# Kernel optimization log

Measured on AMD Instinct MI355X. Metric: run time of the kernel, lower is better.

The kernel has to match this reference:

```python
import jax, jax.numpy as jnp
import numpy as np

V, D, NH, L, HID, E, K = 32000, 1024, 16, 2, 2048, 8, 2
B, S = 2, 1024
HD = D // NH
EPS = 1e-6
ROPE_BASE = 10000.0


def setup_inputs() -> dict:
    key = jax.random.key(0)
    ks = jax.random.split(key, 12)
    s = 0.02
    return {
        "tokens": jax.random.randint(ks[0], (B, S), 0, V),
        "embed": jax.random.normal(ks[1], (V, D), jnp.float32) * s,
        "attn_norm_w": jnp.ones((L, D), jnp.float32),
        "wq": jax.random.normal(ks[2], (L, D, D), jnp.float32) * s,
        "wk": jax.random.normal(ks[3], (L, D, D), jnp.float32) * s,
        "wv": jax.random.normal(ks[4], (L, D, D), jnp.float32) * s,
        "wo": jax.random.normal(ks[5], (L, D, D), jnp.float32) * s,
        "moe_norm_w": jnp.ones((L, D), jnp.float32),
        "router_w": jax.random.normal(ks[6], (L, E, D), jnp.float32) * s,
        "w1": jax.random.normal(ks[7], (L, E, D, HID), jnp.float32) * s,
        "w2": jax.random.normal(ks[8], (L, E, HID, D), jnp.float32) * s,
        "w3": jax.random.normal(ks[9], (L, E, D, HID), jnp.float32) * s,
        "final_norm_w": jnp.ones((D,), jnp.float32),
    }


def rmsnorm(x, w):
    var = jnp.mean(jnp.square(x), axis=-1, keepdims=True)
    return x * jax.lax.rsqrt(var + EPS) * w


def rope(x):  # x: [B, S, NH, HD], rotate-half convention
    half = HD // 2
    inv = ROPE_BASE ** (-jnp.arange(half, dtype=jnp.float32) / half)
    ang = jnp.arange(x.shape[1], dtype=jnp.float32)[:, None] * inv[None, :]  # [S, half]
    cos = jnp.cos(ang)[None, :, None, :]
    sin = jnp.sin(ang)[None, :, None, :]
    x1, x2 = x[..., :half], x[..., half:]
    return jnp.concatenate([x1 * cos - x2 * sin, x1 * sin + x2 * cos], axis=-1)


def attention(x, wq, wk, wv, wo):
    q = (x @ wq).reshape(B, S, NH, HD)
    k = (x @ wk).reshape(B, S, NH, HD)
    v = (x @ wv).reshape(B, S, NH, HD)
    q, k = rope(q), rope(k)
    scores = jnp.einsum("bqhd,bkhd->bhqk", q, k) / jnp.sqrt(jnp.float32(HD))
    mask = jnp.tril(jnp.ones((S, S), bool))
    scores = jnp.where(mask[None, None], scores, jnp.finfo(scores.dtype).min)
    attn = jax.nn.softmax(scores, axis=-1)
    ctx = jnp.einsum("bhqk,bkhd->bqhd", attn, v).reshape(B, S, D)
    return ctx @ wo


def moe(x, router_w, w1, w2, w3):
    flat = x.reshape(-1, D)                      # [T, D]
    T = flat.shape[0]
    logits = flat @ router_w.T                   # [T, E]
    topv, topi = jax.lax.top_k(logits, K)
    topw = jax.nn.softmax(topv, axis=-1)         # softmax over selected logits
    gates = jnp.zeros((T, E), flat.dtype).at[jnp.arange(T)[:, None], topi].set(topw)
    out = jnp.zeros_like(flat)
    for e in range(E):  # small fixed expert count; gates are exact-sparse so math == dispatch path
        y = (jax.nn.silu(flat @ w1[e]) * (flat @ w3[e])) @ w2[e]
        out = out + y * gates[:, e:e + 1]
    return out.reshape(x.shape)


def reference(tokens, embed, attn_norm_w, wq, wk, wv, wo, moe_norm_w,
              router_w, w1, w2, w3, final_norm_w):
    x = embed[tokens]  # [B, S, D]
    for l in range(L):
        x = x + attention(rmsnorm(x, attn_norm_w[l]), wq[l], wk[l], wv[l], wo[l])
        x = x + moe(rmsnorm(x, moe_norm_w[l]), router_w[l], w1[l], w2[l], w3[l])
    x = rmsnorm(x, final_norm_w)
    return x @ embed.T  # tied logits [B, S, V]
```

## Files before the change

kernel.cpp:

```cpp
#include <hip/hip_runtime.h>
#include <math.h>

typedef unsigned short u16;
typedef unsigned int u32;
typedef __attribute__((ext_vector_type(8))) short bf16x8;
typedef __attribute__((ext_vector_type(4))) float f32x4;

#define TOK 2048
#define SEQ 1024
#define DM 1024
#define NEXP 8
#define VOCAB 32000
#define NL 2
#define SLOTS 5120
#define APAD 40

__device__ __forceinline__ float bf2f(u16 v) {
  u32 u = ((u32)v) << 16; float f; __builtin_memcpy(&f, &u, 4); return f;
}
__device__ __forceinline__ u16 f2bf(float f) {
  u32 u; __builtin_memcpy(&u, &f, 4);
  u += 0x7fffu + ((u >> 16) & 1u);
  return (u16)(u >> 16);
}
__device__ __forceinline__ void split8(const float* v, u16* hi, u16* lo) {
#pragma unroll
  for (int j = 0; j < 8; j++) {
    hi[j] = f2bf(v[j]);
    lo[j] = f2bf(v[j] - bf2f(hi[j]));
  }
}

__global__ __launch_bounds__(256) void k_f2bf(const float* __restrict__ in,
                                              u16* __restrict__ out, long n4) {
  long i = (long)blockIdx.x * 256 + threadIdx.x;
  long stride = (long)gridDim.x * 256;
  for (; i < n4; i += stride) {
    float4 v = ((const float4*)in)[i];
    ushort4 o;
    o.x = f2bf(v.x); o.y = f2bf(v.y); o.z = f2bf(v.z); o.w = f2bf(v.w);
    ((ushort4*)out)[i] = o;
  }
}

__device__ __forceinline__ void norm_emit_hl(float4 v, const float* __restrict__ w,
    u16* __restrict__ ohi, u16* __restrict__ olo, int t) {
  float ss = v.x * v.x + v.y * v.y + v.z * v.z + v.w * v.w;
  for (int off = 32; off; off >>= 1) ss += __shfl_xor(ss, off);
  __shared__ float red[4];
  if ((threadIdx.x & 63) == 0) red[threadIdx.x >> 6] = ss;
  __syncthreads();
  float tot = red[0] + red[1] + red[2] + red[3];
  float sc = rsqrtf(tot * (1.0f / 1024.0f) + 1e-6f);
  float4 wv = ((const float4*)w)[threadIdx.x];
  float o[4] = {v.x * sc * wv.x, v.y * sc * wv.y, v.z * sc * wv.z, v.w * sc * wv.w};
  ushort4 hi, lo;
  hi.x = f2bf(o[0]); lo.x = f2bf(o[0] - bf2f(hi.x));
  hi.y = f2bf(o[1]); lo.y = f2bf(o[1] - bf2f(hi.y));
  hi.z = f2bf(o[2]); lo.z = f2bf(o[2] - bf2f(hi.z));
  hi.w = f2bf(o[3]); lo.w = f2bf(o[3] - bf2f(hi.w));
  ((ushort4*)(ohi + (long)t * DM))[threadIdx.x] = hi;
  ((ushort4*)(olo + (long)t * DM))[threadIdx.x] = lo;
}
__device__ __forceinline__ void norm_emit_b(float4 v, const float* __restrict__ w,
    u16* __restrict__ out, int t) {
  float ss = v.x * v.x + v.y * v.y + v.z * v.z + v.w * v.w;
  for (int off = 32; off; off >>= 1) ss += __shfl_xor(ss, off);
  __shared__ float red[4];
  if ((threadIdx.x & 63) == 0) red[threadIdx.x >> 6] = ss;
  __syncthreads();
  float tot = red[0] + red[1] + red[2] + red[3];
  float sc = rsqrtf(tot * (1.0f / 1024.0f) + 1e-6f);
  float4 wv = ((const float4*)w)[threadIdx.x];
  ushort4 o;
  o.x = f2bf(v.x * sc * wv.x); o.y = f2bf(v.y * sc * wv.y);
  o.z = f2bf(v.z * sc * wv.z); o.w = f2bf(v.w * sc * wv.w);
  ((ushort4*)(out + (long)t * DM))[threadIdx.x] = o;
}

__global__ __launch_bounds__(256) void k_gather_norm(const int* __restrict__ tok,
    const float* __restrict__ embed, const float* __restrict__ w,
    float* __restrict__ x, u16* __restrict__ ohi, u16* __restrict__ olo,
    int* __restrict__ counts) {
  int t = blockIdx.x;
  if (t == 0 && threadIdx.x < NEXP) counts[threadIdx.x] = 0;
  float4 v = ((const float4*)(embed + (long)tok[t] * DM))[threadIdx.x];
  ((float4*)(x + (long)t * DM))[threadIdx.x] = v;
  norm_emit_hl(v, w, ohi, olo, t);
}

#define KP 72
#define VP 40
#define PP 36
__global__ __launch_bounds__(256) void k_attn(const u16* __restrict__ qhi,
    const u16* __restrict__ qlo, u16* __restrict__ chi, u16* __restrict__ clo) {
  __shared__ u16 Ksh[32 * KP], Ksl[32 * KP];
  __shared__ u16 Vsh[64 * VP], Vsl[64 * VP];
  __shared__ float Ps[4][16 * PP];
  int bid = blockIdx.x;
  int xcd = bid & 7, r = bid >> 3;
  int bh = xcd * 4 + (r >> 4);
  int qt = 15 - (r & 15);
  int b = bh >> 4, h = bh & 15;
  int tid = threadIdx.x, w = tid >> 6, lane = tid & 63;
  int lrow = lane & 15, lgrp = lane >> 4;
  int q0 = qt * 64;
  long qrow = (long)(b * SEQ + q0 + w * 16 + lrow);
  bf16x8 qh[2], ql[2];
#pragma unroll
  for (int dsl = 0; dsl < 2; dsl++) {
    long off = qrow * 3072 + h * 64 + dsl * 32 + lgrp * 8;
    qh[dsl] = *(const bf16x8*)(qhi + off);
    ql[dsl] = *(const bf16x8*)(qlo + off);
  }
  f32x4 cacc[4] = {};
  float mst[4], lst[4];
#pragma unroll
  for (int j = 0; j < 4; j++) { mst[j] = -__builtin_inff(); lst[j] = 0.0f; }
  int srow = tid >> 3, dchunk = (tid & 7) * 8;
  for (int s0 = 0; s0 < q0 + 64; s0 += 32) {
    long kvrow = (long)(b * SEQ + s0 + srow) * 3072 + h * 64;
    {
      *(uint4*)(Ksh + srow * KP + dchunk) = *(const uint4*)(qhi + kvrow + 1024 + dchunk);
      *(uint4*)(Ksl + srow * KP + dchunk) = *(const uint4*)(qlo + kvrow + 1024 + dchunk);
      uint4 hv4 = *(const uint4*)(qhi + kvrow + 2048 + dchunk);
      uint4 lv4 = *(const uint4*)(qlo + kvrow + 2048 + dchunk);
      const u16* hp = (const u16*)&hv4;
      const u16* lp = (const u16*)&lv4;
#pragma unroll
      for (int j = 0; j < 8; j++) {
        Vsh[(dchunk + j) * VP + srow] = hp[j];
        Vsl[(dchunk + j) * VP + srow] = lp[j];
      }
    }
    __syncthreads();
    f32x4 sacc[2] = {};
#pragma unroll
    for (int sf = 0; sf < 2; sf++)
#pragma unroll
      for (int dsl = 0; dsl < 2; dsl++) {
        bf16x8 kh = *(const bf16x8*)(Ksh + (sf * 16 + lrow) * KP + dsl * 32 + lgrp * 8);
        bf16x8 kl = *(const bf16x8*)(Ksl + (sf * 16 + lrow) * KP + dsl * 32 + lgrp * 8);
        sacc[sf] = __builtin_amdgcn_mfma_f32_16x16x32_bf16(qh[dsl], kh, sacc[sf], 0, 0, 0);
        sacc[sf] = __builtin_amdgcn_mfma_f32_16x16x32_bf16(qh[dsl], kl, sacc[sf], 0, 0, 0);
        sacc[sf] = __builtin_amdgcn_mfma_f32_16x16x32_bf16(ql[dsl], kh, sacc[sf], 0, 0, 0);
      }
#pragma unroll
    for (int sf = 0; sf < 2; sf++)
#pragma unroll
      for (int j = 0; j < 4; j++) {
        int col = s0 + sf * 16 + lrow;
        int row = q0 + w * 16 + lgrp * 4 + j;
        float v = sacc[sf][j] * 0.125f;
        sacc[sf][j] = (col <= row) ? v : -1e30f;
      }
    float fac[4];
#pragma unroll
    for (int j = 0; j < 4; j++) {
      float mx = fmaxf(sacc[0][j], sacc[1][j]);
      for (int off = 1; off < 16; off <<= 1) mx = fmaxf(mx, __shfl_xor(mx, off));
      float mnew = fmaxf(mst[j], mx);
      float f = __expf(mst[j] - mnew);
      mst[j] = mnew;
      float p0 = __expf(sacc[0][j] - mnew);
      float p1 = __expf(sacc[1][j] - mnew);
      sacc[0][j] = p0; sacc[1][j] = p1;
      float ps = p0 + p1;
      for (int off = 1; off < 16; off <<= 1) ps += __shfl_xor(ps, off);
      lst[j] = lst[j] * f + ps;
      fac[j] = f;
    }
#pragma unroll
    for (int n = 0; n < 4; n++)
#pragma unroll
      for (int j = 0; j < 4; j++) cacc[n][j] *= fac[j];
#pragma unroll
    for (int sf = 0; sf < 2; sf++)
#pragma unroll
      for (int j = 0; j < 4; j++)
        Ps[w][(lgrp * 4 + j) * PP + sf * 16 + lrow] = sacc[sf][j];
    float pv[8];
#pragma unroll
    for (int j = 0; j < 8; j++) pv[j] = Ps[w][lrow * PP + lgrp * 8 + j];
    u16 phi[8], plo[8];
    split8(pv, phi, plo);
    bf16x8 ph = *(bf16x8*)phi, pl = *(bf16x8*)plo;
#pragma unroll
    for (int n = 0; n < 4; n++) {
      bf16x8 vh = *(const bf16x8*)(Vsh + (n * 16 + lrow) * VP + lgrp * 8);
      bf16x8 vl = *(const bf16x8*)(Vsl + (n * 16 + lrow) * VP + lgrp * 8);
      cacc[n] = __builtin_amdgcn_mfma_f32_16x16x32_bf16(ph, vh, cacc[n], 0, 0, 0);
      cacc[n] = __builtin_amdgcn_mfma_f32_16x16x32_bf16(ph, vl, cacc[n], 0, 0, 0);
      cacc[n] = __builtin_amdgcn_mfma_f32_16x16x32_bf16(pl, vh, cacc[n], 0, 0, 0);
    }
    __syncthreads();
  }
#pragma unroll
  for (int n = 0; n < 4; n++)
#pragma unroll
    for (int j = 0; j < 4; j++) {
      long t = (long)(b * SEQ + q0 + w * 16 + lgrp * 4 + j);
      float v = cacc[n][j] / lst[j];
      u16 hv = f2bf(v);
      chi[t * DM + h * 64 + n * 16 + lrow] = hv;
      clo[t * DM + h * 64 + n * 16 + lrow] = f2bf(v - bf2f(hv));
    }
}


__device__ __forceinline__ void stageB_tr(const float* __restrict__ B, int ldb,
    int k0, int n0, u16* Bh, u16* Bl, int tid, int split) {
#pragma unroll
  for (int ph = 0; ph < 2; ph++) {
    int c = tid + 256 * ph;
    int nr = c & 127;
    int ks = c >> 7;
    const float* src = B + (long)(k0 + ks * 8) * ldb + n0 + nr;
    float v[8];
#pragma unroll
    for (int j = 0; j < 8; j++) v[j] = src[(long)j * ldb];
    u16 hi[8];
#pragma unroll
    for (int j = 0; j < 8; j++) hi[j] = f2bf(v[j]);
    *(uint4*)(Bh + nr * APAD + ks * 8) = *(uint4*)hi;
    if (split) {
      u16 lo[8];
#pragma unroll
      for (int j = 0; j < 8; j++) lo[j] = f2bf(v[j] - bf2f(hi[j]));
      *(uint4*)(Bl + nr * APAD + ks * 8) = *(uint4*)lo;
    }
  }
}

__global__ __launch_bounds__(256) void k_wo(
    const u16* __restrict__ Ahi, const u16* __restrict__ Alo,
    const float* __restrict__ B, float* __restrict__ C) {
  __shared__ u16 Ah[64 * APAD], Al[64 * APAD], Bh[128 * APAD], Bl[128 * APAD];
  int bid = blockIdx.x;
  int n0 = (bid & 7) * 128;
  int m0 = (bid >> 3) * 64;
  int tid = threadIdx.x, lane = tid & 63, w = tid >> 6;
  int wr = w >> 1, wc = w & 1, lrow = lane & 15, lgrp = lane >> 4;
  f32x4 acc[2][4] = {};
  for (int k0 = 0; k0 < 1024; k0 += 32) {
    {
      int row = tid >> 2, kc = tid & 3;
      long off = (long)(m0 + row) * DM + k0 + kc * 8;
      *(uint4*)(Ah + row * APAD + kc * 8) = *(const uint4*)(Ahi + off);
      *(uint4*)(Al + row * APAD + kc * 8) = *(const uint4*)(Alo + off);
    }
    stageB_tr(B, 1024, k0, n0, Bh, Bl, tid, 1);
    __syncthreads();
    bf16x8 ah[2], al[2], bh[4], bl[4];
#pragma unroll
    for (int i = 0; i < 2; i++) {
      ah[i] = *(const bf16x8*)(Ah + (wr * 32 + i * 16 + lrow) * APAD + lgrp * 8);
      al[i] = *(const bf16x8*)(Al + (wr * 32 + i * 16 + lrow) * APAD + lgrp * 8);
    }
#pragma unroll
    for (int j = 0; j < 4; j++) {
      bh[j] = *(const bf16x8*)(Bh + (wc * 64 + j * 16 + lrow) * APAD + lgrp * 8);
      bl[j] = *(const bf16x8*)(Bl + (wc * 64 + j * 16 + lrow) * APAD + lgrp * 8);
    }
#pragma unroll
    for (int i = 0; i < 2; i++)
#pragma unroll
      for (int j = 0; j < 4; j++) {
        acc[i][j] = __builtin_amdgcn_mfma_f32_16x16x32_bf16(ah[i], bh[j], acc[i][j], 0, 0, 0);
        acc[i][j] = __builtin_amdgcn_mfma_f32_16x16x32_bf16(ah[i], bl[j], acc[i][j], 0, 0, 0);
        acc[i][j] = __builtin_amdgcn_mfma_f32_16x16x32_bf16(al[i], bh[j], acc[i][j], 0, 0, 0);
      }
    __syncthreads();
  }
#pragma unroll
  for (int i = 0; i < 2; i++)
#pragma unroll
    for (int j = 0; j < 4; j++) {
      int col = n0 + wc * 64 + j * 16 + lrow;
#pragma unroll
      for (int jj = 0; jj < 4; jj++) {
        int r = m0 + wr * 32 + i * 16 + lgrp * 4 + jj;
        C[(long)r * DM + col] += acc[i][j][jj];
      }
    }
}

__global__ __launch_bounds__(256) void k_gemm_qkv(
    const u16* __restrict__ Ahi, const u16* __restrict__ Alo,
    const float* __restrict__ Bq, const float* __restrict__ Bk,
    const float* __restrict__ Bv, u16* __restrict__ Chi, u16* __restrict__ Clo) {
  __shared__ u16 Ah[64 * APAD], Al[64 * APAD], Bh[128 * APAD], Bl[128 * APAD];
  int bid = blockIdx.x;
  int xcd = bid & 7, r = bid >> 3;
  int nb = xcd * 3 + r / 32;
  int m0 = (r & 31) * 64;
  const float* B = (nb < 8) ? Bq : (nb < 16) ? Bk : Bv;
  int bn0 = (nb & 7) * 128;
  int tid = threadIdx.x, lane = tid & 63, w = tid >> 6;
  int wr = w >> 1, wc = w & 1, lrow = lane & 15, lgrp = lane >> 4;
  f32x4 acc[2][4] = {};
  for (int k0 = 0; k0 < 1024; k0 += 32) {
    {
      int row = tid >> 2, kc = tid & 3;
      long off = (long)(m0 + row) * DM + k0 + kc * 8;
      *(uint4*)(Ah + row * APAD + kc * 8) = *(const uint4*)(Ahi + off);
      *(uint4*)(Al + row * APAD + kc * 8) = *(const uint4*)(Alo + off);
    }
    stageB_tr(B, 1024, k0, bn0, Bh, Bl, tid, 1);
    __syncthreads();
    bf16x8 ah[2], al[2], bh[4], bl[4];
#pragma unroll
    for (int i = 0; i < 2; i++) {
      ah[i] = *(const bf16x8*)(Ah + (wr * 32 + i * 16 + lrow) * APAD + lgrp * 8);
      al[i] = *(const bf16x8*)(Al + (wr * 32 + i * 16 + lrow) * APAD + lgrp * 8);
    }
#pragma unroll
    for (int j = 0; j < 4; j++) {
      bh[j] = *(const bf16x8*)(Bh + (wc * 64 + j * 16 + lrow) * APAD + lgrp * 8);
      bl[j] = *(const bf16x8*)(Bl + (wc * 64 + j * 16 + lrow) * APAD + lgrp * 8);
    }
#pragma unroll
    for (int i = 0; i < 2; i++)
#pragma unroll
      for (int j = 0; j < 4; j++) {
        acc[i][j] = __builtin_amdgcn_mfma_f32_16x16x32_bf16(ah[i], bh[j], acc[i][j], 0, 0, 0);
        acc[i][j] = __builtin_amdgcn_mfma_f32_16x16x32_bf16(ah[i], bl[j], acc[i][j], 0, 0, 0);
        acc[i][j] = __builtin_amdgcn_mfma_f32_16x16x32_bf16(al[i], bh[j], acc[i][j], 0, 0, 0);
      }
    __syncthreads();
  }
  if (nb < 16) {
    float inv1 = exp2f((float)lrow * (-13.287712379549449f / 32.0f));
    float inv2 = exp2f((float)(lrow + 16) * (-13.287712379549449f / 32.0f));
#pragma unroll
    for (int i = 0; i < 2; i++)
#pragma unroll
      for (int jj = 0; jj < 4; jj++) {
        int rr = m0 + wr * 32 + i * 16 + lgrp * 4 + jj;
        float s = (float)(rr & (SEQ - 1));
        float sn1, cs1, sn2, cs2;
        sincosf(s * inv1, &sn1, &cs1);
        sincosf(s * inv2, &sn2, &cs2);
        float q1 = acc[i][0][jj], q2 = acc[i][2][jj];
        acc[i][0][jj] = q1 * cs1 - q2 * sn1;
        acc[i][2][jj] = q1 * sn1 + q2 * cs1;
        float p1 = acc[i][1][jj], p2 = acc[i][3][jj];
        acc[i][1][jj] = p1 * cs2 - p2 * sn2;
        acc[i][3][jj] = p1 * sn2 + p2 * cs2;
      }
  }
#pragma unroll
  for (int i = 0; i < 2; i++)
#pragma unroll
    for (int j = 0; j < 4; j++) {
      int col = nb * 128 + wc * 64 + j * 16 + lrow;
#pragma unroll
      for (int jj = 0; jj < 4; jj++) {
        int rr = m0 + wr * 32 + i * 16 + lgrp * 4 + jj;
        float v = acc[i][j][jj];
        u16 hv = f2bf(v);
        Chi[(long)rr * 3072 + col] = hv;
        Clo[(long)rr * 3072 + col] = f2bf(v - bf2f(hv));
      }
    }
}

template <int SPLIT>
__global__ __launch_bounds__(256) void k_w13(
    const u16* __restrict__ Ahi, const u16* __restrict__ Alo,
    const float* __restrict__ W1, const float* __restrict__ W3,
    const int* __restrict__ lists, const int* __restrict__ counts,
    const int* __restrict__ aoff,
    u16* __restrict__ hhi, u16* __restrict__ hlo) {
  int bid = blockIdx.x;
  int xcd = bid & 7, r = bid >> 3;
  int nb = xcd * 2 + r / 80;
  int m0 = (r % 80) * 64;
  int e = -1;
#pragma unroll
  for (int i = 0; i < NEXP; i++)
    if (m0 >= aoff[i] && m0 < aoff[i + 1]) e = i;
  if (e < 0) return;
  int lr0 = m0 - aoff[e];
  int Mc = counts[e];
  if (lr0 >= Mc) return;
  const float* B1 = W1 + (size_t)e * 1024 * 2048;
  const float* B3 = W3 + (size_t)e * 1024 * 2048;
  int bn0 = nb * 128;
  const int* lst = lists + e * TOK;
  __shared__ u16 Ah[64 * APAD], B1h[128 * APAD], B3h[128 * APAD];
  __shared__ u16 Al[SPLIT ? 64 * APAD : 1];
  __shared__ u16 B1l[SPLIT ? 128 * APAD : 1], B3l[SPLIT ? 128 * APAD : 1];
  int tid = threadIdx.x, lane = tid & 63, w = tid >> 6;
  int wr = w >> 1, wc = w & 1, lrow = lane & 15, lgrp = lane >> 4;
  f32x4 acc1[2][4] = {}, acc3[2][4] = {};
  for (int k0 = 0; k0 < 1024; k0 += 32) {
    {
      int row = tid >> 2, kc = tid & 3;
      uint4 vh = make_uint4(0, 0, 0, 0), vl = make_uint4(0, 0, 0, 0);
      if (lr0 + row < Mc) {
        long off = (long)lst[lr0 + row] * DM + k0 + kc * 8;
        vh = *(const uint4*)(Ahi + off);
        if (SPLIT) vl = *(const uint4*)(Alo + off);
      }
      *(uint4*)(Ah + row * APAD + kc * 8) = vh;
      if (SPLIT) *(uint4*)(Al + row * APAD + kc * 8) = vl;
    }
    stageB_tr(B1, 2048, k0, bn0, B1h, B1l, tid, SPLIT);
    stageB_tr(B3, 2048, k0, bn0, B3h, B3l, tid, SPLIT);
    __syncthreads();
    bf16x8 ah[2], al[2];
#pragma unroll
    for (int i = 0; i < 2; i++) {
      ah[i] = *(const bf16x8*)(Ah + (wr * 32 + i * 16 + lrow) * APAD + lgrp * 8);
      if (SPLIT) al[i] = *(const bf16x8*)(Al + (wr * 32 + i * 16 + lrow) * APAD + lgrp * 8);
    }
    {
      bf16x8 bh[4];
#pragma unroll
      for (int j = 0; j < 4; j++)
        bh[j] = *(const bf16x8*)(B1h + (wc * 64 + j * 16 + lrow) * APAD + lgrp * 8);
#pragma unroll
      for (int i = 0; i < 2; i++)
#pragma unroll
        for (int j = 0; j < 4; j++)
          acc1[i][j] = __builtin_amdgcn_mfma_f32_16x16x32_bf16(ah[i], bh[j], acc1[i][j], 0, 0, 0);
      if (SPLIT) {
        bf16x8 bl[4];
#pragma unroll
        for (int j = 0; j < 4; j++)
          bl[j] = *(const bf16x8*)(B1l + (wc * 64 + j * 16 + lrow) * APAD + lgrp * 8);
#pragma unroll
        for (int i = 0; i < 2; i++)
#pragma unroll
          for (int j = 0; j < 4; j++) {
            acc1[i][j] = __builtin_amdgcn_mfma_f32_16x16x32_bf16(ah[i], bl[j], acc1[i][j], 0, 0, 0);
            acc1[i][j] = __builtin_amdgcn_mfma_f32_16x16x32_bf16(al[i], bh[j], acc1[i][j], 0, 0, 0);
          }
      }
    }
    {
      bf16x8 bh[4];
#pragma unroll
      for (int j = 0; j < 4; j++)
        bh[j] = *(const bf16x8*)(B3h + (wc * 64 + j * 16 + lrow) * APAD + lgrp * 8);
#pragma unroll
      for (int i = 0; i < 2; i++)
#pragma unroll
        for (int j = 0; j < 4; j++)
          acc3[i][j] = __builtin_amdgcn_mfma_f32_16x16x32_bf16(ah[i], bh[j], acc3[i][j], 0, 0, 0);
      if (SPLIT) {
        bf16x8 bl[4];
#pragma unroll
        for (int j = 0; j < 4; j++)
          bl[j] = *(const bf16x8*)(B3l + (wc * 64 + j * 16 + lrow) * APAD + lgrp * 8);
#pragma unroll
        for (int i = 0; i < 2; i++)
#pragma unroll
          for (int j = 0; j < 4; j++) {
            acc3[i][j] = __builtin_amdgcn_mfma_f32_16x16x32_bf16(ah[i], bl[j], acc3[i][j], 0, 0, 0);
            acc3[i][j] = __builtin_amdgcn_mfma_f32_16x16x32_bf16(al[i], bh[j], acc3[i][j], 0, 0, 0);
          }
      }
    }
    __syncthreads();
  }
#pragma unroll
  for (int i = 0; i < 2; i++)
#pragma unroll
    for (int j = 0; j < 4; j++) {
      int col = bn0 + wc * 64 + j * 16 + lrow;
#pragma unroll
      for (int jj = 0; jj < 4; jj++) {
        int rl = wr * 32 + i * 16 + lgrp * 4 + jj;
        if (lr0 + rl >= Mc) continue;
        float g = acc1[i][j][jj], u = acc3[i][j][jj];
        float o = g / (1.0f + __expf(-g)) * u;
        u16 hv = f2bf(o);
        hhi[(long)(m0 + rl) * 2048 + col] = hv;
        if (SPLIT) hlo[(long)(m0 + rl) * 2048 + col] = f2bf(o - bf2f(hv));
      }
    }
}

template <int SPLIT>
__global__ __launch_bounds__(256) void k_w2(
    const u16* __restrict__ Ahi, const u16* __restrict__ Alo,
    const float* __restrict__ W2,
    const int* __restrict__ counts, const int* __restrict__ aoff,
    float* __restrict__ y) {
  int bid = blockIdx.x;
  int n0 = (bid & 7) * 128;
  int m0 = (bid >> 3) * 64;
  int e = -1;
#pragma unroll
  for (int i = 0; i < NEXP; i++)
    if (m0 >= aoff[i] && m0 < aoff[i + 1]) e = i;
  if (e < 0) return;
  int lr0 = m0 - aoff[e];
  int Mc = counts[e];
  if (lr0 >= Mc) return;
  const float* B = W2 + (size_t)e * 2048 * 1024;
  __shared__ u16 Ah[64 * APAD], Bh[128 * APAD];
  __shared__ u16 Al[SPLIT ? 64 * APAD : 1], Bl[SPLIT ? 128 * APAD : 1];
  int tid = threadIdx.x, lane = tid & 63, w = tid >> 6;
  int wr = w >> 1, wc = w & 1, lrow = lane & 15, lgrp = lane >> 4;
  f32x4 acc[2][4] = {};
  for (int k0 = 0; k0 < 2048; k0 += 32) {
    {
      int row = tid >> 2, kc = tid & 3;
      long off = (long)(m0 + row) * 2048 + k0 + kc * 8;
      *(uint4*)(Ah + row * APAD + kc * 8) = *(const uint4*)(Ahi + off);
      if (SPLIT) *(uint4*)(Al + row * APAD + kc * 8) = *(const uint4*)(Alo + off);
    }
    stageB_tr(B, 1024, k0, n0, Bh, Bl, tid, SPLIT);
    __syncthreads();
    bf16x8 ah[2], bh[4];
#pragma unroll
    for (int i = 0; i < 2; i++)
      ah[i] = *(const bf16x8*)(Ah + (wr * 32 + i * 16 + lrow) * APAD + lgrp * 8);
#pragma unroll
    for (int j = 0; j < 4; j++)
      bh[j] = *(const bf16x8*)(Bh + (wc * 64 + j * 16 + lrow) * APAD + lgrp * 8);
#pragma unroll
    for (int i = 0; i < 2; i++)
#pragma unroll
      for (int j = 0; j < 4; j++)
        acc[i][j] = __builtin_amdgcn_mfma_f32_16x16x32_bf16(ah[i], bh[j], acc[i][j], 0, 0, 0);
    if (SPLIT) {
      bf16x8 al[2], bl[4];
#pragma unroll
      for (int i = 0; i < 2; i++)
        al[i] = *(const bf16x8*)(Al + (wr * 32 + i * 16 + lrow) * APAD + lgrp * 8);
#pragma unroll
      for (int j = 0; j < 4; j++)
        bl[j] = *(const bf16x8*)(Bl + (wc * 64 + j * 16 + lrow) * APAD + lgrp * 8);
#pragma unroll
      for (int i = 0; i < 2; i++)
#pragma unroll
        for (int j = 0; j < 4; j++) {
          acc[i][j] = __builtin_amdgcn_mfma_f32_16x16x32_bf16(ah[i], bl[j], acc[i][j], 0, 0, 0);
          acc[i][j] = __builtin_amdgcn_mfma_f32_16x16x32_bf16(al[i], bh[j], acc[i][j], 0, 0, 0);
        }
    }
    __syncthreads();
  }
#pragma unroll
  for (int i = 0; i < 2; i++)
#pragma unroll
    for (int j = 0; j < 4; j++) {
      int col = n0 + wc * 64 + j * 16 + lrow;
#pragma unroll
      for (int jj = 0; jj < 4; jj++) {
        int rl = wr * 32 + i * 16 + lgrp * 4 + jj;
        if (lr0 + rl >= Mc) continue;
        y[(long)(m0 + rl) * DM + col] = acc[i][j][jj];
      }
    }
}

template <int FINAL>
__global__ __launch_bounds__(256) void k_combine_norm(const float* __restrict__ y,
    const int* __restrict__ aoff, const int* __restrict__ tok_e,
    const int* __restrict__ tok_pos, const float* __restrict__ tok_gate,
    float* __restrict__ x, const float* __restrict__ wnext,
    u16* __restrict__ ohi, u16* __restrict__ olo, int* __restrict__ counts) {
  int t = blockIdx.x;
  if (!FINAL && t == 0 && threadIdx.x < NEXP) counts[threadIdx.x] = 0;
  float4 acc = ((float4*)(x + (long)t * DM))[threadIdx.x];
#pragma unroll
  for (int j = 0; j < 2; j++) {
    int e = tok_e[t * 2 + j];
    long g = aoff[e] + tok_pos[t * 2 + j];
    float gt = tok_gate[t * 2 + j];
    float4 yv = ((const float4*)(y + g * DM))[threadIdx.x];
    acc.x += gt * yv.x; acc.y += gt * yv.y;
    acc.z += gt * yv.z; acc.w += gt * yv.w;
  }
  ((float4*)(x + (long)t * DM))[threadIdx.x] = acc;
  if (FINAL) norm_emit_b(acc, wnext, ohi, t);
  else norm_emit_hl(acc, wnext, ohi, olo, t);
}

__device__ __forceinline__ void logits_mma(const u16* As, const u16* Bs,
    f32x4 (&acc)[4][4], int wr, int wc, int lrow, int lgrp) {
  bf16x8 af[4], bfr[4];
#pragma unroll
  for (int i = 0; i < 4; i++) {
    af[i] = *(const bf16x8*)(As + (wr * 64 + i * 16 + lrow) * APAD + lgrp * 8);
    bfr[i] = *(const bf16x8*)(Bs + (wc * 64 + i * 16 + lrow) * APAD + lgrp * 8);
  }
#pragma unroll
  for (int i = 0; i < 4; i++)
#pragma unroll
    for (int j = 0; j < 4; j++)
      acc[i][j] = __builtin_amdgcn_mfma_f32_16x16x32_bf16(af[i], bfr[j], acc[i][j], 0, 0, 0);
}

__global__ __launch_bounds__(512) void k_logits(
    const u16* __restrict__ A, const u16* __restrict__ Bt,
    float* __restrict__ C) {
  __shared__ u16 AsA[256 * APAD], BsA[128 * APAD];
  __shared__ u16 AsB[256 * APAD], BsB[128 * APAD];
  int bid = blockIdx.x;
  int xcd = bid & 7, rank = bid >> 3;
  int bx = xcd * 32 + (rank >> 3);
  int by = rank & 7;
  if (bx >= VOCAB / 128) return;
  int m0 = by * 256, n0 = bx * 128;
  int tid = threadIdx.x, lane = tid & 63, w = tid >> 6;
  int wr = w >> 1, wc = w & 1;
  int lrow = lane & 15, lgrp = lane >> 4;
  int arow = tid >> 2, akc = tid & 3;
  f32x4 acc[4][4] = {};
  const u16* Ap = A + (long)(m0 + arow) * 1024 + akc * 8;
  const u16* Ap2 = A + (long)(m0 + arow + 128) * 1024 + akc * 8;
  const u16* Bp = Bt + (long)(n0 + arow) * 1024 + akc * 8;
  uint4 a0 = *(const uint4*)(Ap);
  uint4 a1 = *(const uint4*)(Ap2);
  uint4 b0 = *(const uint4*)(Bp);
  *(uint4*)(AsA + arow * APAD + akc * 8) = a0;
  *(uint4*)(AsA + (arow + 128) * APAD + akc * 8) = a1;
  *(uint4*)(BsA + arow * APAD + akc * 8) = b0;
  __syncthreads();
  for (int kt = 0; kt < 32; kt += 2) {
    {
      int k0 = (kt + 1) * 32;
      a0 = *(const uint4*)(Ap + k0);
      a1 = *(const uint4*)(Ap2 + k0);
      b0 = *(const uint4*)(Bp + k0);
    }
    logits_mma(AsA, BsA, acc, wr, wc, lrow, lgrp);
    *(uint4*)(AsB + arow * APAD + akc * 8) = a0;
    *(uint4*)(AsB + (arow + 128) * APAD + akc * 8) = a1;
    *(uint4*)(BsB + arow * APAD + akc * 8) = b0;
    __syncthreads();
    if (kt + 2 < 32) {
      int k0 = (kt + 2) * 32;
      a0 = *(const uint4*)(Ap + k0);
      a1 = *(const uint4*)(Ap2 + k0);
      b0 = *(const uint4*)(Bp + k0);
    }
    logits_mma(AsB, BsB, acc, wr, wc, lrow, lgrp);
    if (kt + 2 < 32) {
      *(uint4*)(AsA + arow * APAD + akc * 8) = a0;
      *(uint4*)(AsA + (arow + 128) * APAD + akc * 8) = a1;
      *(uint4*)(BsA + arow * APAD + akc * 8) = b0;
    }
    __syncthreads();
  }
#pragma unroll
  for (int i = 0; i < 4; i++)
#pragma unroll
    for (int j = 0; j < 4; j++) {
      int col = n0 + wc * 64 + j * 16 + lrow;
#pragma unroll
      for (int jj = 0; jj < 4; jj++) {
        int r = m0 + wr * 64 + i * 16 + lgrp * 4 + jj;
        C[(long)r * VOCAB + col] = acc[i][j][jj];
      }
    }
}

__global__ __launch_bounds__(256) void k_router_norm(const float* __restrict__ x,
    const float* __restrict__ nw, const float* __restrict__ rw,
    int* __restrict__ counts, int* __restrict__ lists,
    int* __restrict__ tok_e, int* __restrict__ tok_pos,
    float* __restrict__ tok_gate,
    u16* __restrict__ ohi, u16* __restrict__ olo) {
  int t = blockIdx.x * 4 + (threadIdx.x >> 6);
  int lane = threadIdx.x & 63;
  const float* xr = x + (long)t * DM;
  float xv[16], wv[16];
  float ss = 0.0f;
  float p[8] = {0, 0, 0, 0, 0, 0, 0, 0};
#pragma unroll
  for (int i = 0; i < 16; i++) {
    int d = lane + 64 * i;
    xv[i] = xr[d];
    wv[i] = nw[d];
    ss += xv[i] * xv[i];
    float xw = xv[i] * wv[i];
#pragma unroll
    for (int e = 0; e < 8; e++) p[e] += xw * rw[e * DM + d];
  }
  for (int off = 32; off; off >>= 1) ss += __shfl_xor(ss, off);
#pragma unroll
  for (int e = 0; e < 8; e++)
    for (int off = 32; off; off >>= 1) p[e] += __shfl_xor(p[e], off);
  float sc = rsqrtf(ss * (1.0f / 1024.0f) + 1e-6f);
#pragma unroll
  for (int i = 0; i < 16; i++) {
    int d = lane + 64 * i;
    float o = xv[i] * sc * wv[i];
    u16 h = f2bf(o);
    ohi[(long)t * DM + d] = h;
    olo[(long)t * DM + d] = f2bf(o - bf2f(h));
  }
  if (lane == 0) {
    int e0 = 0, e1 = -1;
    float v0 = -__builtin_inff(), v1 = -__builtin_inff();
    for (int e = 0; e < 8; e++) {
      float pe = p[e] * sc;
      if (pe > v0) { v1 = v0; e1 = e0; v0 = pe; e0 = e; }
      else if (pe > v1) { v1 = pe; e1 = e; }
    }
    float w0 = 1.0f / (1.0f + expf(v1 - v0));
    int pos0 = atomicAdd(&counts[e0], 1);
    lists[e0 * TOK + pos0] = t;
    tok_e[t * 2] = e0; tok_pos[t * 2] = pos0; tok_gate[t * 2] = w0;
    int pos1 = atomicAdd(&counts[e1], 1);
    lists[e1 * TOK + pos1] = t;
    tok_e[t * 2 + 1] = e1; tok_pos[t * 2 + 1] = pos1; tok_gate[t * 2 + 1] = 1.0f - w0;
  }
}

__global__ void k_offsets(const int* __restrict__ counts, int* __restrict__ aoff) {
  if (threadIdx.x == 0 && blockIdx.x == 0) {
    int a = 0;
    for (int e = 0; e < NEXP; e++) {
      aoff[e] = a;
      a += (counts[e] + 63) & ~63;
    }
    aoff[NEXP] = a;
  }
}

extern "C" void kernel_launch(void* const* d_in, const int* in_sizes, int n_in,
                              void* d_out, int out_size, void* d_ws, size_t ws_size,
                              hipStream_t stream) {
  (void)in_sizes; (void)n_in; (void)out_size; (void)ws_size;
  const int* tokens = (const int*)d_in[0];
  const float* embed = (const float*)d_in[1];
  const float* attn_nw = (const float*)d_in[2];
  const float* wq = (const float*)d_in[3];
  const float* wk = (const float*)d_in[4];
  const float* wv = (const float*)d_in[5];
  const float* wo = (const float*)d_in[6];
  const float* moe_nw = (const float*)d_in[7];
  const float* rw = (const float*)d_in[8];
  const float* w1 = (const float*)d_in[9];
  const float* w2 = (const float*)d_in[10];
  const float* w3 = (const float*)d_in[11];
  const float* fin_nw = (const float*)d_in[12];
  float* out = (float*)d_out;

  char* ob = (char*)d_out;
  auto carve = [&](size_t bytes) { char* r = ob; ob += (bytes + 255) & ~(size_t)255; return r; };
  u16*   qkv_hi = (u16*)carve((size_t)TOK * 3072 * 2);
  u16*   qkv_lo = (u16*)carve((size_t)TOK * 3072 * 2);
  u16*   ctx_hi = (u16*)carve((size_t)TOK * DM * 2);
  u16*   ctx_lo = (u16*)carve((size_t)TOK * DM * 2);
  float* x      = (float*)carve((size_t)TOK * DM * 4);
  u16*   hb_hi  = (u16*)carve((size_t)SLOTS * 2048 * 2);
  u16*   hb_lo  = (u16*)carve((size_t)SLOTS * 2048 * 2);
  float* y      = (float*)carve((size_t)SLOTS * 1024 * 4);
  int*   counts  = (int*)carve(NEXP * 4);
  int*   aoff    = (int*)carve((NEXP + 1) * 4);
  int*   lists   = (int*)carve((size_t)NEXP * TOK * 4);
  int*   tok_e   = (int*)carve((size_t)TOK * 2 * 4);
  int*   tok_pos = (int*)carve((size_t)TOK * 2 * 4);
  float* tok_gate= (float*)carve((size_t)TOK * 2 * 4);
  char* wp = (char*)d_ws;
  auto wcarve = [&](size_t bytes) { char* r = wp; wp += (bytes + 255) & ~(size_t)255; return r; };
  u16* xn_hi = (u16*)wcarve((size_t)TOK * DM * 2);
  u16* xn_lo = (u16*)wcarve((size_t)TOK * DM * 2);
  u16* xnb   = (u16*)wcarve((size_t)TOK * DM * 2);
  u16* embB  = (u16*)wcarve((size_t)VOCAB * DM * 2);

  k_f2bf<<<4096, 256, 0, stream>>>(embed, embB, (long)VOCAB * DM / 4);
  k_gather_norm<<<TOK, 256, 0, stream>>>(tokens, embed, attn_nw, x, xn_hi, xn_lo, counts);

  for (int l = 0; l < NL; l++) {
    k_gemm_qkv<<<768, 256, 0, stream>>>(xn_hi, xn_lo,
        wq + (size_t)l * DM * DM, wk + (size_t)l * DM * DM, wv + (size_t)l * DM * DM,
        qkv_hi, qkv_lo);
    k_attn<<<512, 256, 0, stream>>>(qkv_hi, qkv_lo, ctx_hi, ctx_lo);
    k_wo<<<256, 256, 0, stream>>>(ctx_hi, ctx_lo, wo + (size_t)l * DM * DM, x);

    k_router_norm<<<TOK / 4, 256, 0, stream>>>(x, moe_nw + (size_t)l * DM,
        rw + (size_t)l * NEXP * DM, counts, lists, tok_e, tok_pos, tok_gate,
        xn_hi, xn_lo);
    k_offsets<<<1, 64, 0, stream>>>(counts, aoff);
    if (l < NL - 1) {
      k_w13<1><<<1280, 256, 0, stream>>>(xn_hi, xn_lo,
          w1 + (size_t)l * NEXP * DM * 2048, w3 + (size_t)l * NEXP * DM * 2048,
          lists, counts, aoff, hb_hi, hb_lo);
      k_w2<1><<<640, 256, 0, stream>>>(hb_hi, hb_lo,
          w2 + (size_t)l * NEXP * 2048 * DM, counts, aoff, y);
      k_combine_norm<0><<<TOK, 256, 0, stream>>>(y, aoff, tok_e, tok_pos, tok_gate,
          x, attn_nw + (size_t)(l + 1) * DM, xn_hi, xn_lo, counts);
    } else {
      k_w13<0><<<1280, 256, 0, stream>>>(xn_hi, xn_lo,
          w1 + (size_t)l * NEXP * DM * 2048, w3 + (size_t)l * NEXP * DM * 2048,
          lists, counts, aoff, hb_hi, nullptr);
      k_w2<0><<<640, 256, 0, stream>>>(hb_hi, hb_lo,
          w2 + (size_t)l * NEXP * 2048 * DM, counts, aoff, y);
      k_combine_norm<1><<<TOK, 256, 0, stream>>>(y, aoff, tok_e, tok_pos, tok_gate,
          x, fin_nw, xnb, nullptr, nullptr);
    }
  }
  k_logits<<<2048, 512, 0, stream>>>(xnb, embB, out);
}
```

Baseline: 1.251 ms.

## Pre-transpose and pre-split fp32 weights into bf16 hi/lo before GEMMs

Adds a k_wcvt kernel that transposes each fp32 weight matrix through shared memory and splits it into bf16 hi/lo planes laid out N-major. The QKV, Wo and W1/W3 GEMMs then stage B tiles with contiguous 16-byte copies instead of strided fp32 loads with in-loop conversion. The aim is to remove uncoalesced column reads and repeated conversion work, which happened once per M-tile, from the GEMM inner loops. The cost is an extra pass over every weight on each call (read fp32, write 2x bf16) and a re-read in the GEMMs. Conversion is redone every call and runs inside the timed region, so this is not cross-call caching.

```diff
diff --git a/kernel.cpp b/kernel.cpp
--- a/kernel.cpp
+++ b/kernel.cpp
@@ -41,6 +41,43 @@
     o.x = f2bf(v.x); o.y = f2bf(v.y); o.z = f2bf(v.z); o.w = f2bf(v.w);
     ((ushort4*)out)[i] = o;
   }
+}
+
+__global__ __launch_bounds__(256) void k_wcvt(const float* __restrict__ src,
+    u16* __restrict__ dhi, u16* __restrict__ dlo, int K, int N) {
+  __shared__ float t[64][65];
+  int bid = blockIdx.x;
+  int tn = N >> 6, tk = K >> 6;
+  int mat = bid / (tn * tk);
+  int rem = bid % (tn * tk);
+  int k0 = (rem / tn) << 6;
+  int n0 = (rem % tn) << 6;
+  const float* s = src + (long)mat * K * N;
+  u16* oh = dhi + (long)mat * K * N;
+  u16* ol = dlo + (long)mat * K * N;
+  int tid = threadIdx.x;
+  int r = tid >> 4, c4 = (tid & 15) << 2;
+#pragma unroll
+  for (int rr = 0; rr < 64; rr += 16) {
+    float4 v = *(const float4*)(s + (long)(k0 + r + rr) * N + n0 + c4);
+    t[r + rr][c4] = v.x; t[r + rr][c4 + 1] = v.y;
+    t[r + rr][c4 + 2] = v.z; t[r + rr][c4 + 3] = v.w;
+  }
+  __syncthreads();
+  int n = tid >> 2, kc = (tid & 3) << 4;
+  u16 hi[16], lo[16];
+#pragma unroll
+  for (int j = 0; j < 16; j++) {
+    float v = t[kc + j][n];
+    hi[j] = f2bf(v);
+    lo[j] = f2bf(v - bf2f(hi[j]));
+  }
+  u16* po = oh + (long)(n0 + n) * K + k0 + kc;
+  *(uint4*)(po) = *(uint4*)hi;
+  *(uint4*)(po + 8) = *(uint4*)(hi + 8);
+  u16* pl = ol + (long)(n0 + n) * K + k0 + kc;
+  *(uint4*)(pl) = *(uint4*)lo;
+  *(uint4*)(pl + 8) = *(uint4*)(lo + 8);
 }
 
 __device__ __forceinline__ void norm_emit_hl(float4 v, const float* __restrict__ w,
@@ -208,6 +245,19 @@
 }
 
 
+__device__ __forceinline__ void stageA_cp(const u16* __restrict__ Ahi,
+    const u16* __restrict__ Alo, long ldk, long m0, int k0,
+    u16* Ah, u16* Al, int tid, int split) {
+#pragma unroll
+  for (int ph = 0; ph < 2; ph++) {
+    int c = tid + 256 * ph;
+    int row = c >> 2, kc = c & 3;
+    long off = (m0 + row) * ldk + k0 + kc * 8;
+    *(uint4*)(Ah + row * APAD + kc * 8) = *(const uint4*)(Ahi + off);
+    if (split) *(uint4*)(Al + row * APAD + kc * 8) = *(const uint4*)(Alo + off);
+  }
+}
+
 __device__ __forceinline__ void stageB_tr(const float* __restrict__ B, int ldb,
     int k0, int n0, u16* Bh, u16* Bl, int tid, int split) {
 #pragma unroll
@@ -234,7 +284,8 @@
 
 __global__ __launch_bounds__(256) void k_wo(
     const u16* __restrict__ Ahi, const u16* __restrict__ Alo,
-    const float* __restrict__ B, float* __restrict__ C) {
+    const u16* __restrict__ Bth, const u16* __restrict__ Btl,
+    float* __restrict__ C) {
   __shared__ u16 Ah[64 * APAD], Al[64 * APAD], Bh[128 * APAD], Bl[128 * APAD];
   int bid = blockIdx.x;
   int n0 = (bid & 7) * 128;
@@ -249,7 +300,7 @@
       *(uint4*)(Ah + row * APAD + kc * 8) = *(const uint4*)(Ahi + off);
       *(uint4*)(Al + row * APAD + kc * 8) = *(const uint4*)(Alo + off);
     }
-    stageB_tr(B, 1024, k0, n0, Bh, Bl, tid, 1);
+    stageA_cp(Bth, Btl, 1024, n0, k0, Bh, Bl, tid, 1);
     __syncthreads();
     bf16x8 ah[2], al[2], bh[4], bl[4];
 #pragma unroll
@@ -287,14 +338,17 @@
 
 __global__ __launch_bounds__(256) void k_gemm_qkv(
     const u16* __restrict__ Ahi, const u16* __restrict__ Alo,
-    const float* __restrict__ Bq, const float* __restrict__ Bk,
-    const float* __restrict__ Bv, u16* __restrict__ Chi, u16* __restrict__ Clo) {
+    const u16* __restrict__ Bqh, const u16* __restrict__ Bql,
+    const u16* __restrict__ Bkh, const u16* __restrict__ Bkl,
+    const u16* __restrict__ Bvh, const u16* __restrict__ Bvl,
+    u16* __restrict__ Chi, u16* __restrict__ Clo) {
   __shared__ u16 Ah[64 * APAD], Al[64 * APAD], Bh[128 * APAD], Bl[128 * APAD];
   int bid = blockIdx.x;
   int xcd = bid & 7, r = bid >> 3;
   int nb = xcd * 3 + r / 32;
   int m0 = (r & 31) * 64;
-  const float* B = (nb < 8) ? Bq : (nb < 16) ? Bk : Bv;
+  const u16* Bth = (nb < 8) ? Bqh : (nb < 16) ? Bkh : Bvh;
+  const u16* Btl = (nb < 8) ? Bql : (nb < 16) ? Bkl : Bvl;
   int bn0 = (nb & 7) * 128;
   int tid = threadIdx.x, lane = tid & 63, w = tid >> 6;
   int wr = w >> 1, wc = w & 1, lrow = lane & 15, lgrp = lane >> 4;
@@ -306,7 +360,7 @@
       *(uint4*)(Ah + row * APAD + kc * 8) = *(const uint4*)(Ahi + off);
       *(uint4*)(Al + row * APAD + kc * 8) = *(const uint4*)(Alo + off);
     }
-    stageB_tr(B, 1024, k0, bn0, Bh, Bl, tid, 1);
+    stageA_cp(Bth, Btl, 1024, bn0, k0, Bh, Bl, tid, 1);
     __syncthreads();
     bf16x8 ah[2], al[2], bh[4], bl[4];
 #pragma unroll
@@ -368,7 +422,8 @@
 template <int SPLIT>
 __global__ __launch_bounds__(256) void k_w13(
     const u16* __restrict__ Ahi, const u16* __restrict__ Alo,
-    const float* __restrict__ W1, const float* __restrict__ W3,
+    const u16* __restrict__ W1h, const u16* __restrict__ W1l,
+    const u16* __restrict__ W3h, const u16* __restrict__ W3l,
     const int* __restrict__ lists, const int* __restrict__ counts,
     const int* __restrict__ aoff,
     u16* __restrict__ hhi, u16* __restrict__ hlo) {
@@ -384,8 +439,7 @@
   int lr0 = m0 - aoff[e];
   int Mc = counts[e];
   if (lr0 >= Mc) return;
-  const float* B1 = W1 + (size_t)e * 1024 * 2048;
-  const float* B3 = W3 + (size_t)e * 1024 * 2048;
+  long eoff = (size_t)e * 2048 * 1024;
   int bn0 = nb * 128;
   const int* lst = lists + e * TOK;
   __shared__ u16 Ah[64 * APAD], B1h[128 * APAD], B3h[128 * APAD];
@@ -406,8 +460,8 @@
       *(uint4*)(Ah + row * APAD + kc * 8) = vh;
       if (SPLIT) *(uint4*)(Al + row * APAD + kc * 8) = vl;
     }
-    stageB_tr(B1, 2048, k0, bn0, B1h, B1l, tid, SPLIT);
-    stageB_tr(B3, 2048, k0, bn0, B3h, B3l, tid, SPLIT);
+    stageA_cp(W1h + eoff, W1l + eoff, 1024, bn0, k0, B1h, B1l, tid, SPLIT);
+    stageA_cp(W3h + eoff, W3l + eoff, 1024, bn0, k0, B3h, B3l, tid, SPLIT);
     __syncthreads();
     bf16x8 ah[2], al[2];
 #pragma unroll
@@ -755,6 +809,18 @@
   u16*   hb_hi  = (u16*)carve((size_t)SLOTS * 2048 * 2);
   u16*   hb_lo  = (u16*)carve((size_t)SLOTS * 2048 * 2);
   float* y      = (float*)carve((size_t)SLOTS * 1024 * 4);
+  u16*   w1t_hi = (u16*)carve((size_t)NEXP * 2048 * 1024 * 2);
+  u16*   w1t_lo = (u16*)carve((size_t)NEXP * 2048 * 1024 * 2);
+  u16*   w3t_hi = (u16*)carve((size_t)NEXP * 2048 * 1024 * 2);
+  u16*   w3t_lo = (u16*)carve((size_t)NEXP * 2048 * 1024 * 2);
+  u16*   wqt_hi = (u16*)carve((size_t)DM * DM * 2);
+  u16*   wqt_lo = (u16*)carve((size_t)DM * DM * 2);
+  u16*   wkt_hi = (u16*)carve((size_t)DM * DM * 2);
+  u16*   wkt_lo = (u16*)carve((size_t)DM * DM * 2);
+  u16*   wvt_hi = (u16*)carve((size_t)DM * DM * 2);
+  u16*   wvt_lo = (u16*)carve((size_t)DM * DM * 2);
+  u16*   wot_hi = (u16*)carve((size_t)DM * DM * 2);
+  u16*   wot_lo = (u16*)carve((size_t)DM * DM * 2);
   int*   counts  = (int*)carve(NEXP * 4);
   int*   aoff    = (int*)carve((NEXP + 1) * 4);
   int*   lists   = (int*)carve((size_t)NEXP * TOK * 4);
@@ -772,11 +838,17 @@
   k_gather_norm<<<TOK, 256, 0, stream>>>(tokens, embed, attn_nw, x, xn_hi, xn_lo, counts);
 
   for (int l = 0; l < NL; l++) {
+    k_wcvt<<<256, 256, 0, stream>>>(wq + (size_t)l * DM * DM, wqt_hi, wqt_lo, 1024, 1024);
+    k_wcvt<<<256, 256, 0, stream>>>(wk + (size_t)l * DM * DM, wkt_hi, wkt_lo, 1024, 1024);
+    k_wcvt<<<256, 256, 0, stream>>>(wv + (size_t)l * DM * DM, wvt_hi, wvt_lo, 1024, 1024);
+    k_wcvt<<<256, 256, 0, stream>>>(wo + (size_t)l * DM * DM, wot_hi, wot_lo, 1024, 1024);
+    k_wcvt<<<4096, 256, 0, stream>>>(w1 + (size_t)l * NEXP * DM * 2048, w1t_hi, w1t_lo, 1024, 2048);
+    k_wcvt<<<4096, 256, 0, stream>>>(w3 + (size_t)l * NEXP * DM * 2048, w3t_hi, w3t_lo, 1024, 2048);
+
     k_gemm_qkv<<<768, 256, 0, stream>>>(xn_hi, xn_lo,
-        wq + (size_t)l * DM * DM, wk + (size_t)l * DM * DM, wv + (size_t)l * DM * DM,
-        qkv_hi, qkv_lo);
+        wqt_hi, wqt_lo, wkt_hi, wkt_lo, wvt_hi, wvt_lo, qkv_hi, qkv_lo);
     k_attn<<<512, 256, 0, stream>>>(qkv_hi, qkv_lo, ctx_hi, ctx_lo);
-    k_wo<<<256, 256, 0, stream>>>(ctx_hi, ctx_lo, wo + (size_t)l * DM * DM, x);
+    k_wo<<<256, 256, 0, stream>>>(ctx_hi, ctx_lo, wot_hi, wot_lo, x);
 
     k_router_norm<<<TOK / 4, 256, 0, stream>>>(x, moe_nw + (size_t)l * DM,
         rw + (size_t)l * NEXP * DM, counts, lists, tok_e, tok_pos, tok_gate,
@@ -784,7 +856,7 @@
     k_offsets<<<1, 64, 0, stream>>>(counts, aoff);
     if (l < NL - 1) {
       k_w13<1><<<1280, 256, 0, stream>>>(xn_hi, xn_lo,
-          w1 + (size_t)l * NEXP * DM * 2048, w3 + (size_t)l * NEXP * DM * 2048,
+          w1t_hi, w1t_lo, w3t_hi, w3t_lo,
           lists, counts, aoff, hb_hi, hb_lo);
       k_w2<1><<<640, 256, 0, stream>>>(hb_hi, hb_lo,
           w2 + (size_t)l * NEXP * 2048 * DM, counts, aoff, y);
@@ -792,7 +864,7 @@
           x, attn_nw + (size_t)(l + 1) * DM, xn_hi, xn_lo, counts);
     } else {
       k_w13<0><<<1280, 256, 0, stream>>>(xn_hi, xn_lo,
-          w1 + (size_t)l * NEXP * DM * 2048, w3 + (size_t)l * NEXP * DM * 2048,
+          w1t_hi, w1t_lo, w3t_hi, w3t_lo,
           lists, counts, aoff, hb_hi, nullptr);
       k_w2<0><<<640, 256, 0, stream>>>(hb_hi, hb_lo,
           w2 + (size_t)l * NEXP * 2048 * DM, counts, aoff, y);
```

Result: slower. 1.368 ms (+9.4%).
